# Optimization experiments

Measured on AMD Instinct MI355X. Metric: run time of the kernel, lower is better.

The kernel has to match this reference:

```python
import jax, jax.numpy as jnp
import numpy as np

T, B, H, O = 512, 64, 512, 128
G = 4 * H  # PyTorch gate order: i, f, g, o


def setup_inputs() -> dict:
    key = jax.random.key(0)
    ks = jax.random.split(key, 10)
    s = 1.0 / np.sqrt(H)
    return {
        "x": jax.random.normal(ks[0], (T, B, H), jnp.float32),
        "h0": jnp.zeros((1, B, H), jnp.float32),
        "c0": jnp.zeros((1, B, H), jnp.float32),
        "W_ih1": jax.random.normal(ks[1], (G, H), jnp.float32) * s,
        "W_hh1": jax.random.normal(ks[2], (G, H), jnp.float32) * s,
        "b_ih1": jax.random.normal(ks[3], (G,), jnp.float32) * s,
        "b_hh1": jax.random.normal(ks[4], (G,), jnp.float32) * s,
        "W_ih2": jax.random.normal(ks[5], (G, H), jnp.float32) * s,
        "W_hh2": jax.random.normal(ks[6], (G, H), jnp.float32) * s,
        "b_ih2": jax.random.normal(ks[7], (G,), jnp.float32) * s,
        "b_hh2": jax.random.normal(ks[8], (G,), jnp.float32) * s,
        "W_out": jax.random.normal(ks[9], (O, H), jnp.float32) * s,
        "b_out": jnp.zeros((O,), jnp.float32),
    }


def _lstm_layer(x, h0, c0, W_ih, W_hh, b_ih, b_hh):
    # x: [T,B,H]; h0,c0: [B,H]. PyTorch LSTM math, gate order i,f,g,o.
    xg = jnp.einsum('tbh,gh->tbg', x, W_ih) + b_ih + b_hh  # [T,B,4H]
    W_hh_T = W_hh.T

    def step(carry, xg_t):
        h, c = carry
        g = xg_t + h @ W_hh_T
        i, f, gc, o = jnp.split(g, 4, axis=-1)
        i = jax.nn.sigmoid(i)
        f = jax.nn.sigmoid(f)
        gc = jnp.tanh(gc)
        o = jax.nn.sigmoid(o)
        c = f * c + i * gc
        h = o * jnp.tanh(c)
        return (h, c), h

    (hT, cT), ys = jax.lax.scan(step, (h0, c0), xg)
    return ys, hT, cT


def reference(x, h0, c0, W_ih1, W_hh1, b_ih1, b_hh1, W_ih2, W_hh2, b_ih2, b_hh2, W_out, b_out):
    y1, h1, c1 = _lstm_layer(x, h0[0], c0[0], W_ih1, W_hh1, b_ih1, b_hh1)
    # Faithful quirk: lstm2 is initialized with lstm1's FINAL (h, c).
    y2, h2, c2 = _lstm_layer(y1, h1, c1, W_ih2, W_hh2, b_ih2, b_hh2)
    out = y2[-1] @ W_out.T + b_out  # Linear on last timestep; LogSoftmax is unused in forward
    return out, h2[None], c2[None]
```

## Files before the change

kernel.cpp:

```cpp
#include <hip/hip_runtime.h>

typedef unsigned short u16;
typedef unsigned int u32;
typedef unsigned long long u64;
using f32x4 = __attribute__((ext_vector_type(4))) float;
using s16x8 = __attribute__((ext_vector_type(8))) short;
using u32x4 = __attribute__((ext_vector_type(4))) unsigned int;
using u64x2 = __attribute__((ext_vector_type(2))) unsigned long long;

constexpr int Tn = 512, Bn = 64, Hn = 512, Gn = 2048, On = 128;
constexpr int NS = 16;
constexpr int NG = 4;

constexpr size_t HT_BYTES = (size_t)(Tn + 1) * Bn * Hn * 2;
constexpr size_t XG_BYTES = (size_t)Tn * (size_t)Gn * Bn * 2;
constexpr size_t OFF_CMID = 0;
constexpr size_t OFF_HMID = OFF_CMID + (size_t)Bn * Hn * 4;
constexpr size_t OFF_HT1  = OFF_HMID + (size_t)Bn * Hn * 4;
constexpr size_t OFF_XG   = OFF_HT1 + HT_BYTES;

__device__ __forceinline__ u16 f2b(float f) {
  union { float f; unsigned u; } v; v.f = f;
  unsigned r = v.u + 0x7fffu + ((v.u >> 16) & 1u);
  return (u16)(r >> 16);
}
__device__ __forceinline__ float b2f(u16 u) {
  union { unsigned u; float f; } v; v.u = ((unsigned)u) << 16; return v.f;
}
__device__ __forceinline__ s16x8 pack8(float4 lo, float4 hi) {
  s16x8 r;
  r[0] = (short)f2b(lo.x); r[1] = (short)f2b(lo.y); r[2] = (short)f2b(lo.z); r[3] = (short)f2b(lo.w);
  r[4] = (short)f2b(hi.x); r[5] = (short)f2b(hi.y); r[6] = (short)f2b(hi.z); r[7] = (short)f2b(hi.w);
  return r;
}
__device__ __forceinline__ float sigm(float x) {
  float e = __builtin_amdgcn_exp2f(-1.4426950408889634f * x);
  return __builtin_amdgcn_rcpf(1.0f + e);
}
__device__ __forceinline__ float tanh_(float x) {
  float e = __builtin_amdgcn_exp2f(-2.885390081777927f * x);
  return __builtin_amdgcn_rcpf(1.0f + e) * 2.0f - 1.0f;
}
__device__ __forceinline__ u64 ld64_sc(const u64* p) {
  return __hip_atomic_load(p, __ATOMIC_RELAXED, __HIP_MEMORY_SCOPE_AGENT);
}
__device__ __forceinline__ void st64_sc(u64* p, u64 v) {
  __hip_atomic_store(p, v, __ATOMIC_RELAXED, __HIP_MEMORY_SCOPE_AGENT);
}
__device__ __forceinline__ ushort4 u64_to_us4(u64 q) { union { u64 q; ushort4 v; } u; u.q = q; return u.v; }
__device__ __forceinline__ s16x8 u32x4_to_s16x8(u32x4 a) { union { u32x4 a; s16x8 v; } u; u.a = a; return u.v; }

template<bool AF32, bool POLLA>
__device__ __forceinline__ void proj_core(
    const int wg, const int nwg, const void* __restrict__ Ap,
    const float* __restrict__ W, const float* __restrict__ bih,
    const float* __restrict__ bhh, u16* __restrict__ xg)
{
  const int lane = threadIdx.x & 63, wave = threadIdx.x >> 6;
  const int lrow = lane & 15, lk8 = (lane >> 4) << 3;
  for (int tile = wg; tile < 4096; tile += nwg) {
    const int m0 = (tile >> 4) * 128 + (wave & 1) * 64;
    const int n0 = (tile & 15) * 128 + (wave >> 1) * 64;
    f32x4 acc[4][4] = {};
    for (int ks = 0; ks < 16; ++ks) {
      const int k0 = ks * 32 + lk8;
      s16x8 af[4], bfr[4];
      if constexpr (AF32) {
#pragma unroll
        for (int mt = 0; mt < 4; ++mt) {
          const float* ap = (const float*)Ap + (size_t)(m0 + mt * 16 + lrow) * Hn + k0;
          float4 lo = *(const float4*)ap, hi = *(const float4*)(ap + 4);
          af[mt] = pack8(lo, hi);
        }
      } else {
        u32x4 a4[4];
        const char* pa0 = (const char*)((const u16*)Ap + (size_t)(m0 + 0 * 16 + lrow) * Hn + k0);
        const char* pa1 = (const char*)((const u16*)Ap + (size_t)(m0 + 1 * 16 + lrow) * Hn + k0);
        const char* pa2 = (const char*)((const u16*)Ap + (size_t)(m0 + 2 * 16 + lrow) * Hn + k0);
        const char* pa3 = (const char*)((const u16*)Ap + (size_t)(m0 + 3 * 16 + lrow) * Hn + k0);
        asm volatile("global_load_dwordx4 %0, %1, off sc1" : "=v"(a4[0]) : "v"(pa0) : "memory");
        asm volatile("global_load_dwordx4 %0, %1, off sc1" : "=v"(a4[1]) : "v"(pa1) : "memory");
        asm volatile("global_load_dwordx4 %0, %1, off sc1" : "=v"(a4[2]) : "v"(pa2) : "memory");
        asm volatile("global_load_dwordx4 %0, %1, off sc1" : "=v"(a4[3]) : "v"(pa3) : "memory");
        asm volatile("s_waitcnt vmcnt(0)" ::: "memory");
        while (true) {
          bool bad = false;
#pragma unroll
          for (int mt = 0; mt < 4; ++mt)
#pragma unroll
            for (int d = 0; d < 4; ++d) bad = bad | (a4[mt][d] == 0xFFFFFFFFu);
          if (!bad) break;
          __builtin_amdgcn_s_sleep(8);
          asm volatile("global_load_dwordx4 %0, %1, off sc1" : "=v"(a4[0]) : "v"(pa0) : "memory");
          asm volatile("global_load_dwordx4 %0, %1, off sc1" : "=v"(a4[1]) : "v"(pa1) : "memory");
          asm volatile("global_load_dwordx4 %0, %1, off sc1" : "=v"(a4[2]) : "v"(pa2) : "memory");
          asm volatile("global_load_dwordx4 %0, %1, off sc1" : "=v"(a4[3]) : "v"(pa3) : "memory");
          asm volatile("s_waitcnt vmcnt(0)" ::: "memory");
        }
#pragma unroll
        for (int mt = 0; mt < 4; ++mt) af[mt] = u32x4_to_s16x8(a4[mt]);
      }
#pragma unroll
      for (int nt = 0; nt < 4; ++nt) {
        const float* wp = W + (size_t)(n0 + nt * 16 + lrow) * Hn + k0;
        float4 lo = *(const float4*)wp, hi = *(const float4*)(wp + 4);
        bfr[nt] = pack8(lo, hi);
      }
#pragma unroll
      for (int mt = 0; mt < 4; ++mt)
#pragma unroll
        for (int nt = 0; nt < 4; ++nt)
          acc[mt][nt] = __builtin_amdgcn_mfma_f32_16x16x32_bf16(af[mt], bfr[nt], acc[mt][nt], 0, 0, 0);
    }
    const int rbase = (lane >> 4) << 2;
#pragma unroll
    for (int nt = 0; nt < 4; ++nt) {
      const int n = n0 + nt * 16 + lrow;
      const float bias = bih[n] + bhh[n];
#pragma unroll
      for (int mt = 0; mt < 4; ++mt) {
        const int m = m0 + mt * 16 + rbase;
        const int t = m >> 6, b = m & 63;
        const u64 pv = (u64)f2b(acc[mt][nt][0] + bias)
                     | ((u64)f2b(acc[mt][nt][1] + bias) << 16)
                     | ((u64)f2b(acc[mt][nt][2] + bias) << 32)
                     | ((u64)f2b(acc[mt][nt][3] + bias) << 48);
        st64_sc((u64*)(xg + ((size_t)t * Gn + n) * Bn + b), pv);
      }
    }
  }
}

template<bool POLL_XG>
__device__ __forceinline__ void scan_core(
    const int wgid, const u16* __restrict__ xg, const float* __restrict__ Whh,
    const float* __restrict__ hinit, const float* __restrict__ cinit,
    u16* __restrict__ ht, float* __restrict__ h_fin, float* __restrict__ c_fin)
{
  const int g = wgid >> 4, s = wgid & (NS - 1);
  const int tid = threadIdx.x;
  const int lane = tid & 63, w = tid >> 6;
  const int x16 = lane & 15, grp = lane >> 4;
  const int jj = x16 & 7;
  const int j0 = s * 32 + w * 8;
  const int brow = g * 16;
  const int bth = brow + grp * 4;

  __shared__ char hlds[16 * 1024];
  __shared__ u16 hstage[16][32];

  const size_t grow0 = (size_t)(x16 >> 3) * Hn + j0 + jj;
  const size_t grow1 = (size_t)(2 + (x16 >> 3)) * Hn + j0 + jj;
  s16x8 bwh[2][16];
#pragma unroll
  for (int nt = 0; nt < 2; ++nt) {
    const size_t grow = nt ? grow1 : grow0;
#pragma unroll
    for (int ks = 0; ks < 16; ++ks) {
      const float* wp = Whh + grow * Hn + ks * 32 + grp * 8;
      float4 lo = *(const float4*)wp, hi = *(const float4*)(wp + 4);
      bwh[nt][ks] = pack8(lo, hi);
    }
  }

  float c[4];
#pragma unroll
  for (int r = 0; r < 4; ++r) c[r] = cinit[(size_t)(bth + r) * Hn + j0 + jj];

  if (tid < 128) {
    const int row = tid >> 3, cq = tid & 7;
    const float* hp = hinit + (size_t)(brow + row) * Hn + s * 32 + cq * 4;
    u64 v = (u64)f2b(hp[0]) | ((u64)f2b(hp[1]) << 16)
          | ((u64)f2b(hp[2]) << 32) | ((u64)f2b(hp[3]) << 48);
    st64_sc((u64*)(ht + (size_t)(brow + row) * Hn + s * 32 + cq * 4), v);
  }

  ushort4 xv0, xv1;
  {
    const u16* xa = xg + grow0 * Bn + bth;
    const u16* xb = xg + grow1 * Bn + bth;
    if constexpr (POLL_XG) {
      u64 a = ld64_sc((const u64*)xa), b = ld64_sc((const u64*)xb);
      while (a == ~0ull || b == ~0ull) {
        __builtin_amdgcn_s_sleep(2);
        if (a == ~0ull) a = ld64_sc((const u64*)xa);
        if (b == ~0ull) b = ld64_sc((const u64*)xb);
      }
      xv0 = u64_to_us4(a); xv1 = u64_to_us4(b);
    } else {
      xv0 = *(const ushort4*)xa; xv1 = *(const ushort4*)xb;
    }
  }

  for (int t = 0; t < Tn; ++t) {
    const u16* rt = ht + (size_t)t * Bn * Hn;
    const u64* p0 = (const u64*)(rt + (size_t)(brow + (tid >> 6)) * Hn) + ((tid & 63) << 1);
    u64 v[8];
#pragma unroll
    for (int i = 0; i < 4; ++i) {
      v[2 * i]     = ld64_sc(p0 + i * 512);
      v[2 * i + 1] = ld64_sc(p0 + i * 512 + 1);
    }
    while (true) {
      bool all = true;
#pragma unroll
      for (int i = 0; i < 8; ++i) all = all && (v[i] != ~0ull);
      if (all) break;
      __builtin_amdgcn_s_sleep(1);
#pragma unroll
      for (int i = 0; i < 4; ++i) {
        if (v[2 * i]     == ~0ull) v[2 * i]     = ld64_sc(p0 + i * 512);
        if (v[2 * i + 1] == ~0ull) v[2 * i + 1] = ld64_sc(p0 + i * 512 + 1);
      }
    }
    {
      const int row = tid >> 6, ci = tid & 63;
#pragma unroll
      for (int i = 0; i < 4; ++i) {
        const int rr = row + 4 * i;
        u64x2 q; q[0] = v[2 * i]; q[1] = v[2 * i + 1];
        *(u64x2*)(hlds + rr * 1024 + ((ci ^ (rr & 7)) * 16)) = q;
      }
    }
    __syncthreads();
    f32x4 acc0, acc1;
    acc0[0] = b2f(xv0.x); acc0[1] = b2f(xv0.y); acc0[2] = b2f(xv0.z); acc0[3] = b2f(xv0.w);
    acc1[0] = b2f(xv1.x); acc1[1] = b2f(xv1.y); acc1[2] = b2f(xv1.z); acc1[3] = b2f(xv1.w);
#pragma unroll
    for (int ks = 0; ks < 16; ++ks) {
      const s16x8 a = *(const s16x8*)(hlds + x16 * 1024 + ((((ks << 2) + grp) ^ jj) * 16));
      acc0 = __builtin_amdgcn_mfma_f32_16x16x32_bf16(a, bwh[0][ks], acc0, 0, 0, 0);
      acc1 = __builtin_amdgcn_mfma_f32_16x16x32_bf16(a, bwh[1][ks], acc1, 0, 0, 0);
    }
    float hv[4];
#pragma unroll
    for (int r = 0; r < 4; ++r) {
      const float p0v = acc0[r], p1v = acc1[r];
      const float q0 = __shfl_xor(p0v, 8, 64);
      const float q1 = __shfl_xor(p1v, 8, 64);
      const bool lo = (x16 < 8);
      const float gi = lo ? p0v : q0;
      const float gf = lo ? q0 : p0v;
      const float gg = lo ? p1v : q1;
      const float go = lo ? q1 : p1v;
      const float cn = sigm(gf) * c[r] + sigm(gi) * tanh_(gg);
      c[r] = cn;
      hv[r] = sigm(go) * tanh_(cn);
    }
    if (t == Tn - 1 && x16 < 8) {
#pragma unroll
      for (int r = 0; r < 4; ++r) {
        h_fin[(size_t)(bth + r) * Hn + j0 + jj] = hv[r];
        c_fin[(size_t)(bth + r) * Hn + j0 + jj] = c[r];
      }
    }
    {
      float a0 = hv[0], a1 = hv[1], a2 = hv[2], a3 = hv[3];
      const int p = x16 & 3;
      float tvu;
      tvu = (p & 1) ? a0 : a1;  tvu = __shfl_xor(tvu, 1, 64);
      if (p & 1) a0 = tvu; else a1 = tvu;
      tvu = (p & 1) ? a2 : a3;  tvu = __shfl_xor(tvu, 1, 64);
      if (p & 1) a2 = tvu; else a3 = tvu;
      tvu = (p & 2) ? a0 : a2;  tvu = __shfl_xor(tvu, 2, 64);
      if (p & 2) a0 = tvu; else a2 = tvu;
      tvu = (p & 2) ? a1 : a3;  tvu = __shfl_xor(tvu, 2, 64);
      if (p & 2) a1 = tvu; else a3 = tvu;
      if (x16 < 8) {
        const int cc = (x16 >> 2) & 1;
        const u64 yv = (u64)f2b(a0) | ((u64)f2b(a1) << 16)
                     | ((u64)f2b(a2) << 32) | ((u64)f2b(a3) << 48);
        *(u64*)&hstage[grp * 4 + p][w * 8 + cc * 4] = yv;
      }
    }
    __syncthreads();
    if (!(tid & 1)) {
      const int q = tid >> 1, row = q >> 3, cq = q & 7;
      const u64 yv = *(const u64*)&hstage[row][cq * 4];
      st64_sc((u64*)(ht + (size_t)(t + 1) * Bn * Hn + (size_t)(brow + row) * Hn + s * 32 + cq * 4), yv);
    }
    const int tn2 = (t + 1 < Tn) ? t + 1 : t;
    {
      const u16* xa = xg + ((size_t)tn2 * Gn + grow0) * Bn + bth;
      const u16* xb = xg + ((size_t)tn2 * Gn + grow1) * Bn + bth;
      if constexpr (POLL_XG) {
        u64 a = ld64_sc((const u64*)xa), b = ld64_sc((const u64*)xb);
        while (a == ~0ull || b == ~0ull) {
          __builtin_amdgcn_s_sleep(2);
          if (a == ~0ull) a = ld64_sc((const u64*)xa);
          if (b == ~0ull) b = ld64_sc((const u64*)xb);
        }
        xv0 = u64_to_us4(a); xv1 = u64_to_us4(b);
      } else {
        xv0 = *(const ushort4*)xa; xv1 = *(const ushort4*)xb;
      }
    }
    __syncthreads();
  }
}

__global__ __launch_bounds__(256, 1)
void mega_full(const float* __restrict__ x,
               const float* __restrict__ Wih1, const float* __restrict__ bih1, const float* __restrict__ bhh1,
               const float* __restrict__ Whh1, const float* __restrict__ h0, const float* __restrict__ c0,
               u16* __restrict__ ht1, u16* __restrict__ xg,
               const float* __restrict__ Wih2, const float* __restrict__ bih2, const float* __restrict__ bhh2,
               float* __restrict__ h_mid, float* __restrict__ c_mid)
{
  const int bid = blockIdx.x;
  if (bid < 64)
    scan_core<true>(bid, xg, Whh1, h0, c0, ht1, h_mid, c_mid);
  else if (bid < 160)
    proj_core<true, false>(bid - 64, 96, x, Wih1, bih1, bhh1, xg);
  else
    proj_core<false, true>(bid - 160, 96, ht1 + (size_t)Bn * Hn, Wih2, bih2, bhh2, xg);
}

__global__ __launch_bounds__(256, 1)
void scan_plain(const u16* __restrict__ xg, const float* __restrict__ Whh,
                const float* __restrict__ hinit, const float* __restrict__ cinit,
                u16* __restrict__ ht, float* __restrict__ h_fin, float* __restrict__ c_fin)
{
  scan_core<false>(blockIdx.x, xg, Whh, hinit, cinit, ht, h_fin, c_fin);
}

__global__ __launch_bounds__(128)
void out_kernel(const float* __restrict__ h2, const float* __restrict__ Wout,
                const float* __restrict__ bout, float* __restrict__ out)
{
  const int b = blockIdx.x, o = threadIdx.x;
  const float4* hp = (const float4*)(h2 + (size_t)b * Hn);
  const float4* wp = (const float4*)(Wout + (size_t)o * Hn);
  float acc = 0.f;
#pragma unroll 4
  for (int k = 0; k < Hn / 4; ++k) {
    float4 h4 = hp[k], w4 = wp[k];
    acc += h4.x * w4.x + h4.y * w4.y + h4.z * w4.z + h4.w * w4.w;
  }
  out[(size_t)b * On + o] = acc + bout[o];
}

extern "C" void kernel_launch(void* const* d_in, const int* in_sizes, int n_in,
                              void* d_out, int out_size, void* d_ws, size_t ws_size,
                              hipStream_t stream) {
  const float* x     = (const float*)d_in[0];
  const float* h0    = (const float*)d_in[1];
  const float* c0    = (const float*)d_in[2];
  const float* W_ih1 = (const float*)d_in[3];
  const float* W_hh1 = (const float*)d_in[4];
  const float* b_ih1 = (const float*)d_in[5];
  const float* b_hh1 = (const float*)d_in[6];
  const float* W_ih2 = (const float*)d_in[7];
  const float* W_hh2 = (const float*)d_in[8];
  const float* b_ih2 = (const float*)d_in[9];
  const float* b_hh2 = (const float*)d_in[10];
  const float* W_out = (const float*)d_in[11];
  const float* b_out = (const float*)d_in[12];

  float* out    = (float*)d_out;
  float* h2_out = out + (size_t)Bn * On;
  float* c2_out = h2_out + (size_t)Bn * Hn;

  char* w = (char*)d_ws;
  float* c_mid = (float*)(w + OFF_CMID);
  float* h_mid = (float*)(w + OFF_HMID);
  u16*   ht1   = (u16*)(w + OFF_HT1);
  u16*   xg    = (u16*)(w + OFF_XG);

  hipMemsetAsync(ht1, 0xFF, HT_BYTES, stream);
  hipMemsetAsync(xg, 0xFF, XG_BYTES, stream);

  mega_full<<<256, 256, 0, stream>>>(x, W_ih1, b_ih1, b_hh1, W_hh1, h0, c0,
                                     ht1, xg, W_ih2, b_ih2, b_hh2, h_mid, c_mid);
  hipMemsetAsync(ht1, 0xFF, HT_BYTES, stream);
  scan_plain<<<NG * NS, 256, 0, stream>>>(xg, W_hh2, h_mid, c_mid, ht1, h2_out, c2_out);
  out_kernel<<<Bn, 128, 0, stream>>>(h2_out, W_out, b_out, out);
}
```

Measured before the change: 2.642 ms.

## Stage projection A row-blocks in swizzled LDS and reuse across all N tiles

The input-projection workers now load a 128-row block of the A operand once into shared memory, stored as bf16 with an XOR swizzle, and then loop over all 16 N tiles reading A from LDS. Previously each 128x128 output tile reloaded and repacked A from global memory. For the layer-2 projection the readiness polling on ht1 is done once per row block with 64-bit atomic loads, instead of once per k-step. The change also grows the mega kernel's shared allocation to 128 KB, which is shared with the scan blocks. The cost is coarser work units: 256 row blocks spread over 96 workgroups, which may unbalance the load, and the layer-2 projection cannot start on a block until its whole chunk is ready.

```diff
diff --git a/kernel.cpp b/kernel.cpp
--- a/kernel.cpp
+++ b/kernel.cpp
@@ -48,86 +48,102 @@
   __hip_atomic_store(p, v, __ATOMIC_RELAXED, __HIP_MEMORY_SCOPE_AGENT);
 }
 __device__ __forceinline__ ushort4 u64_to_us4(u64 q) { union { u64 q; ushort4 v; } u; u.q = q; return u.v; }
-__device__ __forceinline__ s16x8 u32x4_to_s16x8(u32x4 a) { union { u32x4 a; s16x8 v; } u; u.a = a; return u.v; }
-
-template<bool AF32, bool POLLA>
+
+template<bool AF32>
 __device__ __forceinline__ void proj_core(
     const int wg, const int nwg, const void* __restrict__ Ap,
     const float* __restrict__ W, const float* __restrict__ bih,
-    const float* __restrict__ bhh, u16* __restrict__ xg)
-{
-  const int lane = threadIdx.x & 63, wave = threadIdx.x >> 6;
-  const int lrow = lane & 15, lk8 = (lane >> 4) << 3;
-  for (int tile = wg; tile < 4096; tile += nwg) {
-    const int m0 = (tile >> 4) * 128 + (wave & 1) * 64;
-    const int n0 = (tile & 15) * 128 + (wave >> 1) * 64;
-    f32x4 acc[4][4] = {};
-    for (int ks = 0; ks < 16; ++ks) {
-      const int k0 = ks * 32 + lk8;
-      s16x8 af[4], bfr[4];
-      if constexpr (AF32) {
+    const float* __restrict__ bhh, u16* __restrict__ xg, char* __restrict__ alds)
+{
+  const int tid = threadIdx.x;
+  const int lane = tid & 63, wave = tid >> 6;
+  const int lrow = lane & 15, grp = lane >> 4, lk8 = grp << 3;
+  const int mrow0 = (wave & 1) * 64;
+
+  for (int mb = wg; mb < 256; mb += nwg) {
+    if constexpr (AF32) {
+#pragma unroll 4
+      for (int k = 0; k < 32; ++k) {
+        const int c = tid + k * 256, row = c >> 6, ci = c & 63;
+        const float* ap = (const float*)Ap + (size_t)(mb * 128 + row) * Hn + ci * 8;
+        float4 lo = *(const float4*)ap, hi = *(const float4*)(ap + 4);
+        const s16x8 v = pack8(lo, hi);
+        *(s16x8*)(alds + row * 1024 + ((ci ^ (row & 7)) * 16)) = v;
+      }
+    } else {
+      for (int k = 0; k < 32; k += 8) {
+        u64 va[16];
+#pragma unroll
+        for (int j = 0; j < 8; ++j) {
+          const int c = tid + (k + j) * 256, row = c >> 6, ci = c & 63;
+          const u64* p = (const u64*)((const u16*)Ap + (size_t)(mb * 128 + row) * Hn + ci * 8);
+          va[2 * j] = ld64_sc(p); va[2 * j + 1] = ld64_sc(p + 1);
+        }
+        while (true) {
+          bool all = true;
+#pragma unroll
+          for (int j = 0; j < 16; ++j) all = all && (va[j] != ~0ull);
+          if (all) break;
+          __builtin_amdgcn_s_sleep(8);
+#pragma unroll
+          for (int j = 0; j < 8; ++j) {
+            const int c = tid + (k + j) * 256, row = c >> 6, ci = c & 63;
+            const u64* p = (const u64*)((const u16*)Ap + (size_t)(mb * 128 + row) * Hn + ci * 8);
+            if (va[2 * j]     == ~0ull) va[2 * j]     = ld64_sc(p);
+            if (va[2 * j + 1] == ~0ull) va[2 * j + 1] = ld64_sc(p + 1);
+          }
+        }
+#pragma unroll
+        for (int j = 0; j < 8; ++j) {
+          const int c = tid + (k + j) * 256, row = c >> 6, ci = c & 63;
+          u64x2 q; q[0] = va[2 * j]; q[1] = va[2 * j + 1];
+          *(u64x2*)(alds + row * 1024 + ((ci ^ (row & 7)) * 16)) = q;
+        }
+      }
+    }
+    __syncthreads();
+
+    for (int nb = 0; nb < 16; ++nb) {
+      const int n0 = nb * 128 + (wave >> 1) * 64;
+      f32x4 acc[4][4] = {};
+      for (int ks = 0; ks < 16; ++ks) {
+        const int k0 = ks * 32 + lk8;
+        s16x8 af[4], bfr[4];
 #pragma unroll
         for (int mt = 0; mt < 4; ++mt) {
-          const float* ap = (const float*)Ap + (size_t)(m0 + mt * 16 + lrow) * Hn + k0;
-          float4 lo = *(const float4*)ap, hi = *(const float4*)(ap + 4);
-          af[mt] = pack8(lo, hi);
-        }
-      } else {
-        u32x4 a4[4];
-        const char* pa0 = (const char*)((const u16*)Ap + (size_t)(m0 + 0 * 16 + lrow) * Hn + k0);
-        const char* pa1 = (const char*)((const u16*)Ap + (size_t)(m0 + 1 * 16 + lrow) * Hn + k0);
-        const char* pa2 = (const char*)((const u16*)Ap + (size_t)(m0 + 2 * 16 + lrow) * Hn + k0);
-        const char* pa3 = (const char*)((const u16*)Ap + (size_t)(m0 + 3 * 16 + lrow) * Hn + k0);
-        asm volatile("global_load_dwordx4 %0, %1, off sc1" : "=v"(a4[0]) : "v"(pa0) : "memory");
-        asm volatile("global_load_dwordx4 %0, %1, off sc1" : "=v"(a4[1]) : "v"(pa1) : "memory");
-        asm volatile("global_load_dwordx4 %0, %1, off sc1" : "=v"(a4[2]) : "v"(pa2) : "memory");
-        asm volatile("global_load_dwordx4 %0, %1, off sc1" : "=v"(a4[3]) : "v"(pa3) : "memory");
-        asm volatile("s_waitcnt vmcnt(0)" ::: "memory");
-        while (true) {
-          bool bad = false;
-#pragma unroll
-          for (int mt = 0; mt < 4; ++mt)
-#pragma unroll
-            for (int d = 0; d < 4; ++d) bad = bad | (a4[mt][d] == 0xFFFFFFFFu);
-          if (!bad) break;
-          __builtin_amdgcn_s_sleep(8);
-          asm volatile("global_load_dwordx4 %0, %1, off sc1" : "=v"(a4[0]) : "v"(pa0) : "memory");
-          asm volatile("global_load_dwordx4 %0, %1, off sc1" : "=v"(a4[1]) : "v"(pa1) : "memory");
-          asm volatile("global_load_dwordx4 %0, %1, off sc1" : "=v"(a4[2]) : "v"(pa2) : "memory");
-          asm volatile("global_load_dwordx4 %0, %1, off sc1" : "=v"(a4[3]) : "v"(pa3) : "memory");
-          asm volatile("s_waitcnt vmcnt(0)" ::: "memory");
-        }
-#pragma unroll
-        for (int mt = 0; mt < 4; ++mt) af[mt] = u32x4_to_s16x8(a4[mt]);
-      }
+          const int r = mrow0 + mt * 16 + lrow;
+          af[mt] = *(const s16x8*)(alds + r * 1024 + ((((ks << 2) + grp) ^ (r & 7)) * 16));
+        }
+#pragma unroll
+        for (int nt = 0; nt < 4; ++nt) {
+          const float* wp = W + (size_t)(n0 + nt * 16 + lrow) * Hn + k0;
+          float4 lo = *(const float4*)wp, hi = *(const float4*)(wp + 4);
+          bfr[nt] = pack8(lo, hi);
+        }
+#pragma unroll
+        for (int mt = 0; mt < 4; ++mt)
+#pragma unroll
+          for (int nt = 0; nt < 4; ++nt)
+            acc[mt][nt] = __builtin_amdgcn_mfma_f32_16x16x32_bf16(af[mt], bfr[nt], acc[mt][nt], 0, 0, 0);
+      }
+      const int rbase = grp << 2;
 #pragma unroll
       for (int nt = 0; nt < 4; ++nt) {
-        const float* wp = W + (size_t)(n0 + nt * 16 + lrow) * Hn + k0;
-        float4 lo = *(const float4*)wp, hi = *(const float4*)(wp + 4);
-        bfr[nt] = pack8(lo, hi);
-      }
-#pragma unroll
-      for (int mt = 0; mt < 4; ++mt)
-#pragma unroll
-        for (int nt = 0; nt < 4; ++nt)
-          acc[mt][nt] = __builtin_amdgcn_mfma_f32_16x16x32_bf16(af[mt], bfr[nt], acc[mt][nt], 0, 0, 0);
-    }
-    const int rbase = (lane >> 4) << 2;
-#pragma unroll
-    for (int nt = 0; nt < 4; ++nt) {
-      const int n = n0 + nt * 16 + lrow;
-      const float bias = bih[n] + bhh[n];
-#pragma unroll
-      for (int mt = 0; mt < 4; ++mt) {
-        const int m = m0 + mt * 16 + rbase;
-        const int t = m >> 6, b = m & 63;
-        const u64 pv = (u64)f2b(acc[mt][nt][0] + bias)
-                     | ((u64)f2b(acc[mt][nt][1] + bias) << 16)
-                     | ((u64)f2b(acc[mt][nt][2] + bias) << 32)
-                     | ((u64)f2b(acc[mt][nt][3] + bias) << 48);
-        st64_sc((u64*)(xg + ((size_t)t * Gn + n) * Bn + b), pv);
-      }
-    }
+        const int n = n0 + nt * 16 + lrow;
+        const float bias = bih[n] + bhh[n];
+#pragma unroll
+        for (int mt = 0; mt < 4; ++mt) {
+          const int m = mb * 128 + mrow0 + mt * 16 + rbase;
+          const int t = m >> 6, b = m & 63;
+          const u64 pv = (u64)f2b(acc[mt][nt][0] + bias)
+                       | ((u64)f2b(acc[mt][nt][1] + bias) << 16)
+                       | ((u64)f2b(acc[mt][nt][2] + bias) << 32)
+                       | ((u64)f2b(acc[mt][nt][3] + bias) << 48);
+          st64_sc((u64*)(xg + ((size_t)t * Gn + n) * Bn + b), pv);
+        }
+      }
+    }
+    __syncthreads();
   }
 }
 
@@ -135,7 +151,8 @@
 __device__ __forceinline__ void scan_core(
     const int wgid, const u16* __restrict__ xg, const float* __restrict__ Whh,
     const float* __restrict__ hinit, const float* __restrict__ cinit,
-    u16* __restrict__ ht, float* __restrict__ h_fin, float* __restrict__ c_fin)
+    u16* __restrict__ ht, float* __restrict__ h_fin, float* __restrict__ c_fin,
+    char* __restrict__ smem)
 {
   const int g = wgid >> 4, s = wgid & (NS - 1);
   const int tid = threadIdx.x;
@@ -146,8 +163,8 @@
   const int brow = g * 16;
   const int bth = brow + grp * 4;
 
-  __shared__ char hlds[16 * 1024];
-  __shared__ u16 hstage[16][32];
+  char* hlds = smem;
+  u16 (*hstage)[32] = (u16 (*)[32])(smem + 16384);
 
   const size_t grow0 = (size_t)(x16 >> 3) * Hn + j0 + jj;
   const size_t grow1 = (size_t)(2 + (x16 >> 3)) * Hn + j0 + jj;
@@ -307,13 +324,14 @@
                const float* __restrict__ Wih2, const float* __restrict__ bih2, const float* __restrict__ bhh2,
                float* __restrict__ h_mid, float* __restrict__ c_mid)
 {
+  __shared__ char smem[131072];
   const int bid = blockIdx.x;
   if (bid < 64)
-    scan_core<true>(bid, xg, Whh1, h0, c0, ht1, h_mid, c_mid);
+    scan_core<true>(bid, xg, Whh1, h0, c0, ht1, h_mid, c_mid, smem);
   else if (bid < 160)
-    proj_core<true, false>(bid - 64, 96, x, Wih1, bih1, bhh1, xg);
+    proj_core<true>(bid - 64, 96, x, Wih1, bih1, bhh1, xg, smem);
   else
-    proj_core<false, true>(bid - 160, 96, ht1 + (size_t)Bn * Hn, Wih2, bih2, bhh2, xg);
+    proj_core<false>(bid - 160, 96, ht1 + (size_t)Bn * Hn, Wih2, bih2, bhh2, xg, smem);
 }
 
 __global__ __launch_bounds__(256, 1)
@@ -321,7 +339,8 @@
                 const float* __restrict__ hinit, const float* __restrict__ cinit,
                 u16* __restrict__ ht, float* __restrict__ h_fin, float* __restrict__ c_fin)
 {
-  scan_core<false>(blockIdx.x, xg, Whh, hinit, cinit, ht, h_fin, c_fin);
+  __shared__ char smem[17408];
+  scan_core<false>(blockIdx.x, xg, Whh, hinit, cinit, ht, h_fin, c_fin, smem);
 }
 
 __global__ __launch_bounds__(128)
```

Result: slower. 3.061 ms (+15.9%).

## Gate layer-2 projection on scan progress counters and pre-convert input weights to bf16

Applied to the files above, without the earlier changes.

Each scan workgroup now publishes its completed timestep to a progress array, and the layer-2 projection workgroups wait on those counters before each tile. This replaces the old scheme of reloading A-tiles until no 0xFFFF sentinel words remain. The input-projection weights are also converted to bf16 once by a separate kernel, so the projection loops read packed bf16 directly instead of converting fp32 on every load. The cost is two extra conversion launches and workspace memory, plus a coarser wait that may hold projection tiles back longer than strictly needed.

```diff
diff --git a/kernel.cpp b/kernel.cpp
--- a/kernel.cpp
+++ b/kernel.cpp
@@ -5,7 +5,6 @@
 typedef unsigned long long u64;
 using f32x4 = __attribute__((ext_vector_type(4))) float;
 using s16x8 = __attribute__((ext_vector_type(8))) short;
-using u32x4 = __attribute__((ext_vector_type(4))) unsigned int;
 using u64x2 = __attribute__((ext_vector_type(2))) unsigned long long;
 
 constexpr int Tn = 512, Bn = 64, Hn = 512, Gn = 2048, On = 128;
@@ -14,9 +13,13 @@
 
 constexpr size_t HT_BYTES = (size_t)(Tn + 1) * Bn * Hn * 2;
 constexpr size_t XG_BYTES = (size_t)Tn * (size_t)Gn * Bn * 2;
-constexpr size_t OFF_CMID = 0;
+constexpr size_t WB_BYTES = (size_t)Gn * Hn * 2;
+constexpr size_t OFF_PROG = 0;
+constexpr size_t OFF_CMID = 1024;
 constexpr size_t OFF_HMID = OFF_CMID + (size_t)Bn * Hn * 4;
-constexpr size_t OFF_HT1  = OFF_HMID + (size_t)Bn * Hn * 4;
+constexpr size_t OFF_WB1  = OFF_HMID + (size_t)Bn * Hn * 4;
+constexpr size_t OFF_WB2  = OFF_WB1 + WB_BYTES;
+constexpr size_t OFF_HT1  = OFF_WB2 + WB_BYTES;
 constexpr size_t OFF_XG   = OFF_HT1 + HT_BYTES;
 
 __device__ __forceinline__ u16 f2b(float f) {
@@ -47,20 +50,47 @@
 __device__ __forceinline__ void st64_sc(u64* p, u64 v) {
   __hip_atomic_store(p, v, __ATOMIC_RELAXED, __HIP_MEMORY_SCOPE_AGENT);
 }
+__device__ __forceinline__ u32 ld32_sc(const u32* p) {
+  return __hip_atomic_load(p, __ATOMIC_RELAXED, __HIP_MEMORY_SCOPE_AGENT);
+}
+__device__ __forceinline__ void st32_sc(u32* p, u32 v) {
+  __hip_atomic_store(p, v, __ATOMIC_RELAXED, __HIP_MEMORY_SCOPE_AGENT);
+}
 __device__ __forceinline__ ushort4 u64_to_us4(u64 q) { union { u64 q; ushort4 v; } u; u.q = q; return u.v; }
-__device__ __forceinline__ s16x8 u32x4_to_s16x8(u32x4 a) { union { u32x4 a; s16x8 v; } u; u.a = a; return u.v; }
-
-template<bool AF32, bool POLLA>
+__device__ __forceinline__ s16x8 two_u64_to_s16x8(u64 a, u64 b) {
+  union { u64 q[2]; s16x8 v; } u; u.q[0] = a; u.q[1] = b; return u.v;
+}
+
+__global__ __launch_bounds__(256)
+void cvt_kernel(const float* __restrict__ in, u16* __restrict__ out, int n4) {
+  const int i = blockIdx.x * 256 + threadIdx.x;
+  if (i < n4) {
+    float4 v = ((const float4*)in)[i];
+    ushort4 o; o.x = f2b(v.x); o.y = f2b(v.y); o.z = f2b(v.z); o.w = f2b(v.w);
+    ((ushort4*)out)[i] = o;
+  }
+}
+
+template<bool AF32>
 __device__ __forceinline__ void proj_core(
     const int wg, const int nwg, const void* __restrict__ Ap,
-    const float* __restrict__ W, const float* __restrict__ bih,
-    const float* __restrict__ bhh, u16* __restrict__ xg)
+    const u16* __restrict__ Wb, const float* __restrict__ bih,
+    const float* __restrict__ bhh, u16* __restrict__ xg,
+    volatile u32* __restrict__ prog)
 {
   const int lane = threadIdx.x & 63, wave = threadIdx.x >> 6;
   const int lrow = lane & 15, lk8 = (lane >> 4) << 3;
   for (int tile = wg; tile < 4096; tile += nwg) {
     const int m0 = (tile >> 4) * 128 + (wave & 1) * 64;
     const int n0 = (tile & 15) * 128 + (wave >> 1) * 64;
+    if constexpr (!AF32) {
+      const u32 need = 2u * (u32)(tile >> 4) + 2u;
+      while (true) {
+        const u32 pv = ld32_sc((const u32*)&prog[lane]);
+        if (__all(pv >= need)) break;
+        __builtin_amdgcn_s_sleep(16);
+      }
+    }
     f32x4 acc[4][4] = {};
     for (int ks = 0; ks < 16; ++ks) {
       const int k0 = ks * 32 + lk8;
@@ -73,39 +103,15 @@
           af[mt] = pack8(lo, hi);
         }
       } else {
-        u32x4 a4[4];
-        const char* pa0 = (const char*)((const u16*)Ap + (size_t)(m0 + 0 * 16 + lrow) * Hn + k0);
-        const char* pa1 = (const char*)((const u16*)Ap + (size_t)(m0 + 1 * 16 + lrow) * Hn + k0);
-        const char* pa2 = (const char*)((const u16*)Ap + (size_t)(m0 + 2 * 16 + lrow) * Hn + k0);
-        const char* pa3 = (const char*)((const u16*)Ap + (size_t)(m0 + 3 * 16 + lrow) * Hn + k0);
-        asm volatile("global_load_dwordx4 %0, %1, off sc1" : "=v"(a4[0]) : "v"(pa0) : "memory");
-        asm volatile("global_load_dwordx4 %0, %1, off sc1" : "=v"(a4[1]) : "v"(pa1) : "memory");
-        asm volatile("global_load_dwordx4 %0, %1, off sc1" : "=v"(a4[2]) : "v"(pa2) : "memory");
-        asm volatile("global_load_dwordx4 %0, %1, off sc1" : "=v"(a4[3]) : "v"(pa3) : "memory");
-        asm volatile("s_waitcnt vmcnt(0)" ::: "memory");
-        while (true) {
-          bool bad = false;
-#pragma unroll
-          for (int mt = 0; mt < 4; ++mt)
-#pragma unroll
-            for (int d = 0; d < 4; ++d) bad = bad | (a4[mt][d] == 0xFFFFFFFFu);
-          if (!bad) break;
-          __builtin_amdgcn_s_sleep(8);
-          asm volatile("global_load_dwordx4 %0, %1, off sc1" : "=v"(a4[0]) : "v"(pa0) : "memory");
-          asm volatile("global_load_dwordx4 %0, %1, off sc1" : "=v"(a4[1]) : "v"(pa1) : "memory");
-          asm volatile("global_load_dwordx4 %0, %1, off sc1" : "=v"(a4[2]) : "v"(pa2) : "memory");
-          asm volatile("global_load_dwordx4 %0, %1, off sc1" : "=v"(a4[3]) : "v"(pa3) : "memory");
-          asm volatile("s_waitcnt vmcnt(0)" ::: "memory");
+#pragma unroll
+        for (int mt = 0; mt < 4; ++mt) {
+          const u64* p = (const u64*)((const u16*)Ap + (size_t)(m0 + mt * 16 + lrow) * Hn + k0);
+          af[mt] = two_u64_to_s16x8(ld64_sc(p), ld64_sc(p + 1));
         }
-#pragma unroll
-        for (int mt = 0; mt < 4; ++mt) af[mt] = u32x4_to_s16x8(a4[mt]);
-      }
-#pragma unroll
-      for (int nt = 0; nt < 4; ++nt) {
-        const float* wp = W + (size_t)(n0 + nt * 16 + lrow) * Hn + k0;
-        float4 lo = *(const float4*)wp, hi = *(const float4*)(wp + 4);
-        bfr[nt] = pack8(lo, hi);
-      }
+      }
+#pragma unroll
+      for (int nt = 0; nt < 4; ++nt)
+        bfr[nt] = *(const s16x8*)(Wb + (size_t)(n0 + nt * 16 + lrow) * Hn + k0);
 #pragma unroll
       for (int mt = 0; mt < 4; ++mt)
 #pragma unroll
@@ -135,7 +141,8 @@
 __device__ __forceinline__ void scan_core(
     const int wgid, const u16* __restrict__ xg, const float* __restrict__ Whh,
     const float* __restrict__ hinit, const float* __restrict__ cinit,
-    u16* __restrict__ ht, float* __restrict__ h_fin, float* __restrict__ c_fin)
+    u16* __restrict__ ht, float* __restrict__ h_fin, float* __restrict__ c_fin,
+    u32* __restrict__ prog)
 {
   const int g = wgid >> 4, s = wgid & (NS - 1);
   const int tid = threadIdx.x;
@@ -201,6 +208,7 @@
       v[2 * i]     = ld64_sc(p0 + i * 512);
       v[2 * i + 1] = ld64_sc(p0 + i * 512 + 1);
     }
+    if (prog != nullptr && t > 0 && tid == 0) st32_sc(prog + wgid, (u32)t);
     while (true) {
       bool all = true;
 #pragma unroll
@@ -297,23 +305,24 @@
     }
     __syncthreads();
   }
+  if (prog != nullptr && tid == 0) st32_sc(prog + wgid, (u32)Tn);
 }
 
 __global__ __launch_bounds__(256, 1)
 void mega_full(const float* __restrict__ x,
-               const float* __restrict__ Wih1, const float* __restrict__ bih1, const float* __restrict__ bhh1,
+               const u16* __restrict__ Wb1, const float* __restrict__ bih1, const float* __restrict__ bhh1,
                const float* __restrict__ Whh1, const float* __restrict__ h0, const float* __restrict__ c0,
                u16* __restrict__ ht1, u16* __restrict__ xg,
-               const float* __restrict__ Wih2, const float* __restrict__ bih2, const float* __restrict__ bhh2,
-               float* __restrict__ h_mid, float* __restrict__ c_mid)
+               const u16* __restrict__ Wb2, const float* __restrict__ bih2, const float* __restrict__ bhh2,
+               float* __restrict__ h_mid, float* __restrict__ c_mid, u32* __restrict__ prog)
 {
   const int bid = blockIdx.x;
   if (bid < 64)
-    scan_core<true>(bid, xg, Whh1, h0, c0, ht1, h_mid, c_mid);
+    scan_core<true>(bid, xg, Whh1, h0, c0, ht1, h_mid, c_mid, prog);
   else if (bid < 160)
-    proj_core<true, false>(bid - 64, 96, x, Wih1, bih1, bhh1, xg);
+    proj_core<true>(bid - 64, 96, x, Wb1, bih1, bhh1, xg, nullptr);
   else
-    proj_core<false, true>(bid - 160, 96, ht1 + (size_t)Bn * Hn, Wih2, bih2, bhh2, xg);
+    proj_core<false>(bid - 160, 96, ht1 + (size_t)Bn * Hn, Wb2, bih2, bhh2, xg, prog);
 }
 
 __global__ __launch_bounds__(256, 1)
@@ -321,7 +330,7 @@
                 const float* __restrict__ hinit, const float* __restrict__ cinit,
                 u16* __restrict__ ht, float* __restrict__ h_fin, float* __restrict__ c_fin)
 {
-  scan_core<false>(blockIdx.x, xg, Whh, hinit, cinit, ht, h_fin, c_fin);
+  scan_core<false>(blockIdx.x, xg, Whh, hinit, cinit, ht, h_fin, c_fin, nullptr);
 }
 
 __global__ __launch_bounds__(128)
@@ -362,16 +371,24 @@
   float* c2_out = h2_out + (size_t)Bn * Hn;
 
   char* w = (char*)d_ws;
+  u32*   prog  = (u32*)(w + OFF_PROG);
   float* c_mid = (float*)(w + OFF_CMID);
   float* h_mid = (float*)(w + OFF_HMID);
+  u16*   Wb1   = (u16*)(w + OFF_WB1);
+  u16*   Wb2   = (u16*)(w + OFF_WB2);
   u16*   ht1   = (u16*)(w + OFF_HT1);
   u16*   xg    = (u16*)(w + OFF_XG);
 
+  const int nw4 = Gn * Hn / 4;
+
+  hipMemsetAsync(w, 0, 1024, stream);
   hipMemsetAsync(ht1, 0xFF, HT_BYTES, stream);
   hipMemsetAsync(xg, 0xFF, XG_BYTES, stream);
-
-  mega_full<<<256, 256, 0, stream>>>(x, W_ih1, b_ih1, b_hh1, W_hh1, h0, c0,
-                                     ht1, xg, W_ih2, b_ih2, b_hh2, h_mid, c_mid);
+  cvt_kernel<<<(nw4 + 255) / 256, 256, 0, stream>>>(W_ih1, Wb1, nw4);
+  cvt_kernel<<<(nw4 + 255) / 256, 256, 0, stream>>>(W_ih2, Wb2, nw4);
+
+  mega_full<<<256, 256, 0, stream>>>(x, Wb1, b_ih1, b_hh1, W_hh1, h0, c0,
+                                     ht1, xg, Wb2, b_ih2, b_hh2, h_mid, c_mid, prog);
   hipMemsetAsync(ht1, 0xFF, HT_BYTES, stream);
   scan_plain<<<NG * NS, 256, 0, stream>>>(xg, W_hh2, h_mid, c_mid, ht1, h2_out, c2_out);
   out_kernel<<<Bn, 128, 0, stream>>>(h2_out, W_out, b_out, out);
```

New measurement: 3.492 ms. 1.32x slower.

## Pre-convert input-projection weights to bf16 and double-buffer scan staging to drop a barrier

Applied to the files above, without the earlier changes.

Adds a conversion kernel that turns W_ih1 and W_ih2 into bf16 copies in workspace, so the projection tiles load packed bf16 fragments directly instead of loading fp32 and packing per k-step. This halves weight traffic and removes repeated conversion work in the projection workers. Separately, the scan's h staging buffer is double-buffered by timestep parity, allowing the trailing __syncthreads per step to be removed. The cost is two extra small kernel launches, and the barrier removal relies on the parity buffers preventing write-after-read races across steps. The POLLA template parameter is also dropped.

```diff
diff --git a/kernel.cpp b/kernel.cpp
--- a/kernel.cpp
+++ b/kernel.cpp
@@ -14,9 +14,12 @@
 
 constexpr size_t HT_BYTES = (size_t)(Tn + 1) * Bn * Hn * 2;
 constexpr size_t XG_BYTES = (size_t)Tn * (size_t)Gn * Bn * 2;
+constexpr size_t WB_BYTES = (size_t)Gn * Hn * 2;
 constexpr size_t OFF_CMID = 0;
 constexpr size_t OFF_HMID = OFF_CMID + (size_t)Bn * Hn * 4;
-constexpr size_t OFF_HT1  = OFF_HMID + (size_t)Bn * Hn * 4;
+constexpr size_t OFF_WB1  = OFF_HMID + (size_t)Bn * Hn * 4;
+constexpr size_t OFF_WB2  = OFF_WB1 + WB_BYTES;
+constexpr size_t OFF_HT1  = OFF_WB2 + WB_BYTES;
 constexpr size_t OFF_XG   = OFF_HT1 + HT_BYTES;
 
 __device__ __forceinline__ u16 f2b(float f) {
@@ -50,10 +53,20 @@
 __device__ __forceinline__ ushort4 u64_to_us4(u64 q) { union { u64 q; ushort4 v; } u; u.q = q; return u.v; }
 __device__ __forceinline__ s16x8 u32x4_to_s16x8(u32x4 a) { union { u32x4 a; s16x8 v; } u; u.a = a; return u.v; }
 
-template<bool AF32, bool POLLA>
+__global__ __launch_bounds__(256)
+void cvt_kernel(const float* __restrict__ in, u16* __restrict__ out, int n4) {
+  const int i = blockIdx.x * 256 + threadIdx.x;
+  if (i < n4) {
+    float4 v = ((const float4*)in)[i];
+    ushort4 o; o.x = f2b(v.x); o.y = f2b(v.y); o.z = f2b(v.z); o.w = f2b(v.w);
+    ((ushort4*)out)[i] = o;
+  }
+}
+
+template<bool AF32>
 __device__ __forceinline__ void proj_core(
     const int wg, const int nwg, const void* __restrict__ Ap,
-    const float* __restrict__ W, const float* __restrict__ bih,
+    const u16* __restrict__ Wb, const float* __restrict__ bih,
     const float* __restrict__ bhh, u16* __restrict__ xg)
 {
   const int lane = threadIdx.x & 63, wave = threadIdx.x >> 6;
@@ -101,11 +114,8 @@
         for (int mt = 0; mt < 4; ++mt) af[mt] = u32x4_to_s16x8(a4[mt]);
       }
 #pragma unroll
-      for (int nt = 0; nt < 4; ++nt) {
-        const float* wp = W + (size_t)(n0 + nt * 16 + lrow) * Hn + k0;
-        float4 lo = *(const float4*)wp, hi = *(const float4*)(wp + 4);
-        bfr[nt] = pack8(lo, hi);
-      }
+      for (int nt = 0; nt < 4; ++nt)
+        bfr[nt] = *(const s16x8*)(Wb + (size_t)(n0 + nt * 16 + lrow) * Hn + k0);
 #pragma unroll
       for (int mt = 0; mt < 4; ++mt)
 #pragma unroll
@@ -147,7 +157,7 @@
   const int bth = brow + grp * 4;
 
   __shared__ char hlds[16 * 1024];
-  __shared__ u16 hstage[16][32];
+  __shared__ u16 hstage[2][16][32];
 
   const size_t grow0 = (size_t)(x16 >> 3) * Hn + j0 + jj;
   const size_t grow1 = (size_t)(2 + (x16 >> 3)) * Hn + j0 + jj;
@@ -270,13 +280,13 @@
         const int cc = (x16 >> 2) & 1;
         const u64 yv = (u64)f2b(a0) | ((u64)f2b(a1) << 16)
                      | ((u64)f2b(a2) << 32) | ((u64)f2b(a3) << 48);
-        *(u64*)&hstage[grp * 4 + p][w * 8 + cc * 4] = yv;
+        *(u64*)&hstage[t & 1][grp * 4 + p][w * 8 + cc * 4] = yv;
       }
     }
     __syncthreads();
     if (!(tid & 1)) {
       const int q = tid >> 1, row = q >> 3, cq = q & 7;
-      const u64 yv = *(const u64*)&hstage[row][cq * 4];
+      const u64 yv = *(const u64*)&hstage[t & 1][row][cq * 4];
       st64_sc((u64*)(ht + (size_t)(t + 1) * Bn * Hn + (size_t)(brow + row) * Hn + s * 32 + cq * 4), yv);
     }
     const int tn2 = (t + 1 < Tn) ? t + 1 : t;
@@ -295,25 +305,24 @@
         xv0 = *(const ushort4*)xa; xv1 = *(const ushort4*)xb;
       }
     }
-    __syncthreads();
   }
 }
 
 __global__ __launch_bounds__(256, 1)
 void mega_full(const float* __restrict__ x,
-               const float* __restrict__ Wih1, const float* __restrict__ bih1, const float* __restrict__ bhh1,
+               const u16* __restrict__ Wb1, const float* __restrict__ bih1, const float* __restrict__ bhh1,
                const float* __restrict__ Whh1, const float* __restrict__ h0, const float* __restrict__ c0,
                u16* __restrict__ ht1, u16* __restrict__ xg,
-               const float* __restrict__ Wih2, const float* __restrict__ bih2, const float* __restrict__ bhh2,
+               const u16* __restrict__ Wb2, const float* __restrict__ bih2, const float* __restrict__ bhh2,
                float* __restrict__ h_mid, float* __restrict__ c_mid)
 {
   const int bid = blockIdx.x;
   if (bid < 64)
     scan_core<true>(bid, xg, Whh1, h0, c0, ht1, h_mid, c_mid);
   else if (bid < 160)
-    proj_core<true, false>(bid - 64, 96, x, Wih1, bih1, bhh1, xg);
+    proj_core<true>(bid - 64, 96, x, Wb1, bih1, bhh1, xg);
   else
-    proj_core<false, true>(bid - 160, 96, ht1 + (size_t)Bn * Hn, Wih2, bih2, bhh2, xg);
+    proj_core<false>(bid - 160, 96, ht1 + (size_t)Bn * Hn, Wb2, bih2, bhh2, xg);
 }
 
 __global__ __launch_bounds__(256, 1)
@@ -364,14 +373,20 @@
   char* w = (char*)d_ws;
   float* c_mid = (float*)(w + OFF_CMID);
   float* h_mid = (float*)(w + OFF_HMID);
+  u16*   Wb1   = (u16*)(w + OFF_WB1);
+  u16*   Wb2   = (u16*)(w + OFF_WB2);
   u16*   ht1   = (u16*)(w + OFF_HT1);
   u16*   xg    = (u16*)(w + OFF_XG);
 
+  const int nw4 = Gn * Hn / 4;
+
   hipMemsetAsync(ht1, 0xFF, HT_BYTES, stream);
   hipMemsetAsync(xg, 0xFF, XG_BYTES, stream);
-
-  mega_full<<<256, 256, 0, stream>>>(x, W_ih1, b_ih1, b_hh1, W_hh1, h0, c0,
-                                     ht1, xg, W_ih2, b_ih2, b_hh2, h_mid, c_mid);
+  cvt_kernel<<<(nw4 + 255) / 256, 256, 0, stream>>>(W_ih1, Wb1, nw4);
+  cvt_kernel<<<(nw4 + 255) / 256, 256, 0, stream>>>(W_ih2, Wb2, nw4);
+
+  mega_full<<<256, 256, 0, stream>>>(x, Wb1, b_ih1, b_hh1, W_hh1, h0, c0,
+                                     ht1, xg, Wb2, b_ih2, b_hh2, h_mid, c_mid);
   hipMemsetAsync(ht1, 0xFF, HT_BYTES, stream);
   scan_plain<<<NG * NS, 256, 0, stream>>>(xg, W_hh2, h_mid, c_mid, ht1, h2_out, c2_out);
   out_kernel<<<Bn, 128, 0, stream>>>(h2_out, W_out, b_out, out);
```

After: 2.619 ms, median of 2. No clear change (-0.9%).
